# Kernel optimization log

Measured on AMD Instinct MI355X. Metric: run time of the kernel, lower is better.

## Reference

```python
import jax, jax.numpy as jnp
import numpy as np

B, E = 256, 65536          # batch, embed_dim
S = 256                    # seq_len = sqrt(E)
D = E // S                 # per-token input dim = 256
HID = 512                  # hidden_dim
HD = HID // 2              # per-direction GRU hidden = 256
GH = 128                   # gcn_hidden_dim
K = 5                      # k_neighbors


def setup_inputs() -> dict:
    key = jax.random.key(0)
    ks = jax.random.split(key, 16)
    s = 0.02
    return {
        "C_masked": jax.random.normal(ks[0], (B, E), jnp.float32),
        "W_proj": jax.random.normal(ks[1], (HID, D), jnp.float32) * s,
        "b_proj": jnp.zeros((HID,), jnp.float32),
        "Wih_f": jax.random.normal(ks[2], (3 * HD, HID), jnp.float32) * s,
        "Whh_f": jax.random.normal(ks[3], (3 * HD, HD), jnp.float32) * s,
        "bih_f": jnp.zeros((3 * HD,), jnp.float32),
        "bhh_f": jnp.zeros((3 * HD,), jnp.float32),
        "Wih_b": jax.random.normal(ks[4], (3 * HD, HID), jnp.float32) * s,
        "Whh_b": jax.random.normal(ks[5], (3 * HD, HD), jnp.float32) * s,
        "bih_b": jnp.zeros((3 * HD,), jnp.float32),
        "bhh_b": jnp.zeros((3 * HD,), jnp.float32),
        "W_gcn1": jax.random.normal(ks[6], (HID, GH), jnp.float32) * 0.01,
        "W_gcn2": jax.random.normal(ks[7], (GH, HID), jnp.float32) * 0.01,
    }


def _gru_dir(x, Wih, Whh, bih, bhh, reverse):
    # x: (B, S, IN) -> (B, S, HD). PyTorch GRU cell equations.
    gi = jnp.einsum('bsd,hd->bsh', x, Wih) + bih          # (B,S,3HD)
    gi = jnp.swapaxes(gi, 0, 1)                            # (S,B,3HD)
    h0 = jnp.zeros((x.shape[0], HD), x.dtype)

    def step(h, gi_t):
        gh = h @ Whh.T + bhh
        i_r, i_z, i_n = jnp.split(gi_t, 3, axis=-1)
        h_r, h_z, h_n = jnp.split(gh, 3, axis=-1)
        r = jax.nn.sigmoid(i_r + h_r)
        z = jax.nn.sigmoid(i_z + h_z)
        n = jnp.tanh(i_n + r * h_n)
        h_new = (1.0 - z) * n + z * h
        return h_new, h_new

    _, ys = jax.lax.scan(step, h0, gi, reverse=reverse)    # (S,B,HD), index-aligned
    return jnp.swapaxes(ys, 0, 1)


def reference(C_masked, W_proj, b_proj,
              Wih_f, Whh_f, bih_f, bhh_f,
              Wih_b, Whh_b, bih_b, bhh_b,
              W_gcn1, W_gcn2):
    b, e = C_masked.shape
    s = int(np.sqrt(e))
    d = e // s
    C_seq = C_masked.reshape(b, s, d)
    C_proj = jnp.einsum('bsd,hd->bsh', C_seq, W_proj) + b_proj   # (B,S,HID)

    # BiGRU (eval mode; dropout inactive)
    h_f = _gru_dir(C_proj, Wih_f, Whh_f, bih_f, bhh_f, reverse=False)
    h_b = _gru_dir(C_proj, Wih_b, Whh_b, bih_b, bhh_b, reverse=True)
    H = jnp.concatenate([h_f, h_b], axis=-1)                     # (B,S,HID)

    # KNN graph: cosine sim -> topk -> scatter 1.0 -> add self loops
    Hn = H / jnp.maximum(jnp.linalg.norm(H, axis=-1, keepdims=True), 1e-12)
    sim = jnp.einsum('bnd,bmd->bnm', Hn, Hn)                     # (B,S,S)
    topk_idx = jax.lax.top_k(sim, K)[1]                          # (B,S,K)
    bi = jnp.arange(b)[:, None, None]
    ni = jnp.arange(s)[None, :, None]
    A = jnp.zeros((b, s, s), H.dtype).at[bi, ni, topk_idx].set(1.0)
    A = A + jnp.eye(s, dtype=H.dtype)[None]

    # D^{-1/2} A D^{-1/2}
    deg = A.sum(axis=-1) + 1e-8
    dinv = deg ** -0.5
    A_norm = dinv[:, :, None] * A * dinv[:, None, :]

    # 2-layer GCN (dropout inactive in eval)
    Z1 = jax.nn.relu(jnp.einsum('bnm,bmh->bnh', A_norm, H @ W_gcn1))
    Z = jnp.einsum('bnm,bmh->bnh', A_norm, Z1 @ W_gcn2)
    return Z
```

## Files before the change

kernel.cpp:

```cpp
#include <hip/hip_runtime.h>
#include <hip/hip_fp16.h>
#include <cstdint>
#include <cmath>

typedef _Float16 f16x8 __attribute__((ext_vector_type(8)));
typedef float f32x4 __attribute__((ext_vector_type(4)));

#define MFMA16(A, B, C) __builtin_amdgcn_mfma_f32_16x16x32_f16(A, B, C, 0, 0, 0)
#define LO_SCALE 2048.0f
#define LO_INV   4.8828125e-4f

#define GBM 128
#define GBN 128
#define GBK 16

template<bool TRANSB>
__global__ __launch_bounds__(256)
void gemm_f32(int M, int N, int K,
              const float* __restrict__ A, long long sA,
              const float* __restrict__ B, long long sB,
              float* __restrict__ Cc, long long sC,
              const float* __restrict__ bias,
              const float* __restrict__ rsA,
              const float* __restrict__ rsB)
{
    const int z = blockIdx.z;
    A  += (size_t)z * (size_t)sA;
    B  += (size_t)z * (size_t)sB;
    Cc += (size_t)z * (size_t)sC;

    const int bm = blockIdx.y * GBM;
    const int bn = blockIdx.x * GBN;
    const int tid = threadIdx.x;
    const int tx = tid & 15;
    const int ty = tid >> 4;

    __shared__ float As[GBK][GBM + 4];
    __shared__ float Bs[GBK][GBN + 4];

    float acc[8][8];
#pragma unroll
    for (int i = 0; i < 8; ++i)
#pragma unroll
        for (int j = 0; j < 8; ++j) acc[i][j] = 0.0f;

    const int lr = tid >> 2;
    const int lk = (tid & 3) << 2;
    const int kb_n = tid >> 5;
    const int nb_n = (tid & 31) << 2;

    float sa0 = 1.f, sa1 = 1.f, sb0 = 1.f, sb1 = 1.f;
    if (rsA) {
        sa0 = rsA[(size_t)z * M + bm + lr];
        sa1 = rsA[(size_t)z * M + bm + lr + 64];
    }
    if (TRANSB && rsB) {
        sb0 = rsB[(size_t)z * N + bn + lr];
        sb1 = rsB[(size_t)z * N + bn + lr + 64];
    }

    float4 pa0, pa1, pb0, pb1;

    auto gload = [&](int kt) {
        const float* pA = A + (size_t)(bm + lr) * K + kt * GBK + lk;
        pa0 = *(const float4*)pA;
        pa1 = *(const float4*)(pA + (size_t)64 * K);
        if (TRANSB) {
            const float* pB = B + (size_t)(bn + lr) * K + kt * GBK + lk;
            pb0 = *(const float4*)pB;
            pb1 = *(const float4*)(pB + (size_t)64 * K);
        } else {
            const float* pB = B + (size_t)(kt * GBK + kb_n) * N + bn + nb_n;
            pb0 = *(const float4*)pB;
            pb1 = *(const float4*)(pB + (size_t)8 * N);
        }
    };
    auto sstore = [&]() {
        As[lk + 0][lr] = pa0.x * sa0; As[lk + 1][lr] = pa0.y * sa0;
        As[lk + 2][lr] = pa0.z * sa0; As[lk + 3][lr] = pa0.w * sa0;
        As[lk + 0][lr + 64] = pa1.x * sa1; As[lk + 1][lr + 64] = pa1.y * sa1;
        As[lk + 2][lr + 64] = pa1.z * sa1; As[lk + 3][lr + 64] = pa1.w * sa1;
        if (TRANSB) {
            Bs[lk + 0][lr] = pb0.x * sb0; Bs[lk + 1][lr] = pb0.y * sb0;
            Bs[lk + 2][lr] = pb0.z * sb0; Bs[lk + 3][lr] = pb0.w * sb0;
            Bs[lk + 0][lr + 64] = pb1.x * sb1; Bs[lk + 1][lr + 64] = pb1.y * sb1;
            Bs[lk + 2][lr + 64] = pb1.z * sb1; Bs[lk + 3][lr + 64] = pb1.w * sb1;
        } else {
            *(float4*)&Bs[kb_n][nb_n]     = pb0;
            *(float4*)&Bs[kb_n + 8][nb_n] = pb1;
        }
    };

    const int nkt = K / GBK;
    gload(0);
    sstore();
    __syncthreads();
    for (int kt = 0; kt < nkt; ++kt) {
        if (kt + 1 < nkt) gload(kt + 1);
#pragma unroll
        for (int k = 0; k < GBK; ++k) {
            float4 a0 = *(const float4*)&As[k][ty * 8];
            float4 a1 = *(const float4*)&As[k][ty * 8 + 4];
            float4 b0 = *(const float4*)&Bs[k][tx * 8];
            float4 b1 = *(const float4*)&Bs[k][tx * 8 + 4];
            float av[8] = {a0.x, a0.y, a0.z, a0.w, a1.x, a1.y, a1.z, a1.w};
            float bv[8] = {b0.x, b0.y, b0.z, b0.w, b1.x, b1.y, b1.z, b1.w};
#pragma unroll
            for (int i = 0; i < 8; ++i)
#pragma unroll
                for (int j = 0; j < 8; ++j)
                    acc[i][j] = fmaf(av[i], bv[j], acc[i][j]);
        }
        __syncthreads();
        if (kt + 1 < nkt) { sstore(); __syncthreads(); }
    }

    float bb[8];
#pragma unroll
    for (int j = 0; j < 8; ++j) bb[j] = bias ? bias[bn + tx * 8 + j] : 0.0f;
#pragma unroll
    for (int i = 0; i < 8; ++i) {
        const int row = bm + ty * 8 + i;
        float* cp = Cc + (size_t)row * N + bn + tx * 8;
        float4 o0 = make_float4(acc[i][0] + bb[0], acc[i][1] + bb[1],
                                acc[i][2] + bb[2], acc[i][3] + bb[3]);
        float4 o1 = make_float4(acc[i][4] + bb[4], acc[i][5] + bb[5],
                                acc[i][6] + bb[6], acc[i][7] + bb[7]);
        *(float4*)cp = o0;
        *(float4*)(cp + 4) = o1;
    }
}

__global__ void bias_combine(const float* __restrict__ Wih, const float* __restrict__ b_proj,
                             const float* __restrict__ bih, float* __restrict__ bcomb)
{
    const int j = blockIdx.x * blockDim.x + threadIdx.x;
    if (j >= 768) return;
    float s = bih[j];
    for (int k = 0; k < 512; ++k) s = fmaf(Wih[(size_t)j * 512 + k], b_proj[k], s);
    bcomb[j] = s;
}

__global__ __launch_bounds__(256)
void pack_w(const float* __restrict__ W, unsigned short* __restrict__ pack)
{
    const int idx = blockIdx.x * 256 + threadIdx.x;
    if (idx >= 768 * 256) return;
    const int n = idx >> 8;
    const int k = idx & 255;
    const float w = W[idx];
    const __half hi = __float2half(w);
    const __half lo = __float2half((w - __half2float(hi)) * LO_SCALE);
    const int nt = n >> 4;
    const int lane = ((k >> 3) & 3) * 16 + (n & 15);
    const int j = k & 7;
    const int kc = k >> 5;
    const size_t base = ((size_t)(nt * 8 + kc) * 2) * 512 + lane * 8 + j;
    pack[base]       = __half_as_ushort(hi);
    pack[base + 512] = __half_as_ushort(lo);
}

__global__ __launch_bounds__(256)
void pack_bk(const float* __restrict__ W, unsigned short* __restrict__ pack,
             int K, int N)
{
    const int idx = blockIdx.x * 256 + threadIdx.x;
    if (idx >= K * N) return;
    const int k = idx / N;
    const int n = idx - k * N;
    const float w = W[idx];
    const __half hi = __float2half(w);
    const __half lo = __float2half((w - __half2float(hi)) * LO_SCALE);
    const int nt = n >> 4;
    const int kc = k >> 5;
    const int lane = ((k >> 3) & 3) * 16 + (n & 15);
    const int j = k & 7;
    const int KC = K >> 5;
    const size_t base = ((size_t)(nt * KC + kc) * 2) * 512 + lane * 8 + j;
    pack[base]       = __half_as_ushort(hi);
    pack[base + 512] = __half_as_ushort(lo);
}

__global__ __launch_bounds__(512)
void gi_gemm_c(const float* __restrict__ Cm, const unsigned short* __restrict__ pack,
               const float* __restrict__ bcomb, float* __restrict__ gi, int t0)
{
    const int tid = threadIdx.x;
    const int w = tid >> 6, l = tid & 63;
    const int l15 = l & 15, l4 = l >> 4;
    const int bgrp = blockIdx.x >> 1;
    const int half = blockIdx.x & 1;
    const size_t m0 = (size_t)bgrp * 256 + t0 + half * 64;
    const size_t o0 = (size_t)bgrp * 128 + half * 64;

    __shared__ unsigned short alds[2][64 * 256];

    {
        const int row = tid >> 3;
        const int seg = (tid & 7) * 32;
        const float4* src = (const float4*)(Cm + (m0 + row) * 256 + seg);
        const int sw = (row & 7) << 3;
#pragma unroll
        for (int i = 0; i < 8; ++i) {
            float4 v = src[i];
            float vv[4] = {v.x, v.y, v.z, v.w};
#pragma unroll
            for (int e = 0; e < 4; ++e) {
                const float x = vv[e];
                const __half hi = __float2half(x);
                const __half lo = __float2half((x - __half2float(hi)) * LO_SCALE);
                const int ad = (row << 8) + ((seg + i * 4 + e) ^ sw);
                alds[0][ad] = __half_as_ushort(hi);
                alds[1][ad] = __half_as_ushort(lo);
            }
        }
    }
    __syncthreads();

    const int mt = w >> 1, nh = w & 1;
    f32x4 acc[24];
#pragma unroll
    for (int i = 0; i < 24; ++i) acc[i] = (f32x4){0.f, 0.f, 0.f, 0.f};

    const int ar = mt * 16 + l15;
    const int arow = ar << 8;
    const int asw = (ar & 7) << 3;

#pragma unroll
    for (int kc = 0; kc < 8; ++kc) {
        const int ad = arow + ((kc * 32 + l4 * 8) ^ asw);
        const f16x8 ahi = *(const f16x8*)&alds[0][ad];
        const f16x8 alo = *(const f16x8*)&alds[1][ad];
#pragma unroll
        for (int nt = 0; nt < 24; ++nt) {
            const int nt_lin = nh * 24 + nt;
            const uint4* bp = (const uint4*)(pack + ((size_t)(nt_lin * 8 + kc) * 2) * 512);
            uint4 bh4 = bp[l];
            uint4 bl4 = bp[64 + l];
            const f16x8 Bhi = *reinterpret_cast<const f16x8*>(&bh4);
            const f16x8 Blo = *reinterpret_cast<const f16x8*>(&bl4);
            acc[nt] = MFMA16(ahi, Bhi, acc[nt]);
            f32x4 t2 = (f32x4){0.f, 0.f, 0.f, 0.f};
            t2 = MFMA16(ahi, Blo, t2);
            t2 = MFMA16(alo, Bhi, t2);
#pragma unroll
            for (int r = 0; r < 4; ++r) acc[nt][r] = fmaf(LO_INV, t2[r], acc[nt][r]);
        }
    }

#pragma unroll
    for (int nt = 0; nt < 24; ++nt) {
        const int n = (nh * 24 + nt) * 16 + l15;
        const float bb = bcomb[n];
#pragma unroll
        for (int r = 0; r < 4; ++r) {
            const size_t om = o0 + mt * 16 + l4 * 4 + r;
            __builtin_nontemporal_store(acc[nt][r] + bb, &gi[om * 768 + n]);
        }
    }
}

__global__ __launch_bounds__(1024)
void gru_scan_v8(const float* __restrict__ gi_fc, const float* __restrict__ gi_bc,
                 const float* __restrict__ Whh_f, const float* __restrict__ Whh_b,
                 const float* __restrict__ bhh_f, const float* __restrict__ bhh_b,
                 float* __restrict__ H, float* __restrict__ hstate, int phase)
{
    const int bid = blockIdx.x;
    const int xcd = bid & 7;
    const int dir = xcd >> 2;
    const int grp = (bid >> 3) * 4 + (xcd & 3);
    const float* __restrict__ gi  = dir ? gi_bc : gi_fc;
    const float* __restrict__ Whh = dir ? Whh_b : Whh_f;
    const float* __restrict__ bhh = dir ? bhh_b : bhh_f;
    const int b0 = grp * 4;
    const int t0 = dir ? (128 - phase * 128) : (phase * 128);

    const int tid = threadIdx.x;
    const int j = tid >> 2;
    const int q = tid & 3;

    __shared__ float hb[2][4][256];

    float hreg = (phase == 0)
        ? 0.0f
        : hstate[((size_t)dir * 256 + b0 + q) * 256 + j];
    hb[0][q][j] = hreg;

    const float bh_r = bhh[j], bh_z = bhh[j + 256], bh_n = bhh[j + 512];

    const float* __restrict__ Wr = Whh + (size_t)j * 256 + q * 4;
    const float* __restrict__ Wz = Whh + (size_t)(j + 256) * 256 + q * 4;
    const float* __restrict__ Wn = Whh + (size_t)(j + 512) * 256 + q * 4;

    __syncthreads();

    int p = 0;
    for (int tau = 0; tau < 128; ++tau) {
        const int sc = dir ? (127 - tau) : tau;
        const int tt = t0 + sc;

        const float* gp = gi + ((size_t)(b0 + q) * 128 + sc) * 768 + j;
        const float g_r = __builtin_nontemporal_load(gp);
        const float g_z = __builtin_nontemporal_load(gp + 256);
        const float g_n = __builtin_nontemporal_load(gp + 512);

        float ar0 = 0.f, ar1 = 0.f, ar2 = 0.f, ar3 = 0.f;
        float az0 = 0.f, az1 = 0.f, az2 = 0.f, az3 = 0.f;
        float an0 = 0.f, an1 = 0.f, an2 = 0.f, an3 = 0.f;
#pragma unroll
        for (int u = 0; u < 16; ++u) {
            const float4 wr = *(const float4*)(Wr + u * 16);
            const float4 wz = *(const float4*)(Wz + u * 16);
            const float4 wn = *(const float4*)(Wn + u * 16);
            const int ha = u * 16 + q * 4;
            const float4 h0 = *(const float4*)&hb[p][0][ha];
            const float4 h1 = *(const float4*)&hb[p][1][ha];
            const float4 h2 = *(const float4*)&hb[p][2][ha];
            const float4 h3 = *(const float4*)&hb[p][3][ha];
            ar0 = fmaf(wr.x, h0.x, ar0); ar0 = fmaf(wr.y, h0.y, ar0);
            ar0 = fmaf(wr.z, h0.z, ar0); ar0 = fmaf(wr.w, h0.w, ar0);
            ar1 = fmaf(wr.x, h1.x, ar1); ar1 = fmaf(wr.y, h1.y, ar1);
            ar1 = fmaf(wr.z, h1.z, ar1); ar1 = fmaf(wr.w, h1.w, ar1);
            ar2 = fmaf(wr.x, h2.x, ar2); ar2 = fmaf(wr.y, h2.y, ar2);
            ar2 = fmaf(wr.z, h2.z, ar2); ar2 = fmaf(wr.w, h2.w, ar2);
            ar3 = fmaf(wr.x, h3.x, ar3); ar3 = fmaf(wr.y, h3.y, ar3);
            ar3 = fmaf(wr.z, h3.z, ar3); ar3 = fmaf(wr.w, h3.w, ar3);
            az0 = fmaf(wz.x, h0.x, az0); az0 = fmaf(wz.y, h0.y, az0);
            az0 = fmaf(wz.z, h0.z, az0); az0 = fmaf(wz.w, h0.w, az0);
            az1 = fmaf(wz.x, h1.x, az1); az1 = fmaf(wz.y, h1.y, az1);
            az1 = fmaf(wz.z, h1.z, az1); az1 = fmaf(wz.w, h1.w, az1);
            az2 = fmaf(wz.x, h2.x, az2); az2 = fmaf(wz.y, h2.y, az2);
            az2 = fmaf(wz.z, h2.z, az2); az2 = fmaf(wz.w, h2.w, az2);
            az3 = fmaf(wz.x, h3.x, az3); az3 = fmaf(wz.y, h3.y, az3);
            az3 = fmaf(wz.z, h3.z, az3); az3 = fmaf(wz.w, h3.w, az3);
            an0 = fmaf(wn.x, h0.x, an0); an0 = fmaf(wn.y, h0.y, an0);
            an0 = fmaf(wn.z, h0.z, an0); an0 = fmaf(wn.w, h0.w, an0);
            an1 = fmaf(wn.x, h1.x, an1); an1 = fmaf(wn.y, h1.y, an1);
            an1 = fmaf(wn.z, h1.z, an1); an1 = fmaf(wn.w, h1.w, an1);
            an2 = fmaf(wn.x, h2.x, an2); an2 = fmaf(wn.y, h2.y, an2);
            an2 = fmaf(wn.z, h2.z, an2); an2 = fmaf(wn.w, h2.w, an2);
            an3 = fmaf(wn.x, h3.x, an3); an3 = fmaf(wn.y, h3.y, an3);
            an3 = fmaf(wn.z, h3.z, an3); an3 = fmaf(wn.w, h3.w, an3);
        }

        ar0 += __shfl_xor(ar0, 1); ar0 += __shfl_xor(ar0, 2);
        ar1 += __shfl_xor(ar1, 1); ar1 += __shfl_xor(ar1, 2);
        ar2 += __shfl_xor(ar2, 1); ar2 += __shfl_xor(ar2, 2);
        ar3 += __shfl_xor(ar3, 1); ar3 += __shfl_xor(ar3, 2);
        az0 += __shfl_xor(az0, 1); az0 += __shfl_xor(az0, 2);
        az1 += __shfl_xor(az1, 1); az1 += __shfl_xor(az1, 2);
        az2 += __shfl_xor(az2, 1); az2 += __shfl_xor(az2, 2);
        az3 += __shfl_xor(az3, 1); az3 += __shfl_xor(az3, 2);
        an0 += __shfl_xor(an0, 1); an0 += __shfl_xor(an0, 2);
        an1 += __shfl_xor(an1, 1); an1 += __shfl_xor(an1, 2);
        an2 += __shfl_xor(an2, 1); an2 += __shfl_xor(an2, 2);
        an3 += __shfl_xor(an3, 1); an3 += __shfl_xor(an3, 2);

        const float pr = (q == 0) ? ar0 : (q == 1) ? ar1 : (q == 2) ? ar2 : ar3;
        const float pz = (q == 0) ? az0 : (q == 1) ? az1 : (q == 2) ? az2 : az3;
        const float pn = (q == 0) ? an0 : (q == 1) ? an1 : (q == 2) ? an2 : an3;

        const float rr = 1.0f / (1.0f + expf(-(g_r + pr + bh_r)));
        const float zz = 1.0f / (1.0f + expf(-(g_z + pz + bh_z)));
        const float nn = tanhf(g_n + rr * (pn + bh_n));
        hreg = (1.0f - zz) * nn + zz * hreg;

        hb[p ^ 1][q][j] = hreg;
        __builtin_nontemporal_store(
            hreg, &H[((size_t)(b0 + q) * 256 + tt) * 512 + dir * 256 + j]);
        __syncthreads();
        p ^= 1;
    }

    hstate[((size_t)dir * 256 + b0 + q) * 256 + j] = hreg;
}

__global__ __launch_bounds__(256)
void rownorm(const float* __restrict__ H, float* __restrict__ rinv)
{
    const int row  = blockIdx.x * 4 + (threadIdx.x >> 6);
    const int lane = threadIdx.x & 63;
    const float4* p = (const float4*)(H + (size_t)row * 512);
    float ss = 0.f;
    float4 v = p[lane];
    ss += v.x * v.x + v.y * v.y + v.z * v.z + v.w * v.w;
    v = p[lane + 64];
    ss += v.x * v.x + v.y * v.y + v.z * v.z + v.w * v.w;
#pragma unroll
    for (int off = 32; off >= 1; off >>= 1) ss += __shfl_xor(ss, off);
    if (lane == 0) rinv[row] = 1.0f / fmaxf(sqrtf(ss), 1e-12f);
}

__global__ __launch_bounds__(512)
void sim_mfma(const float* __restrict__ H, const float* __restrict__ rinv,
              float* __restrict__ sim)
{
    const int b = blockIdx.x;
    const int tid = threadIdx.x;
    const int w = tid >> 6, l = tid & 63;
    const int l15 = l & 15, l4 = l >> 4;

    __shared__ unsigned short st[2][256][40];

    f32x4 acc[2][16];
#pragma unroll
    for (int m = 0; m < 2; ++m)
#pragma unroll
        for (int n = 0; n < 16; ++n) acc[m][n] = (f32x4){0.f, 0.f, 0.f, 0.f};

    const int sr = tid >> 1;
    const int sh = (tid & 1) * 16;
    const float rv = rinv[b * 256 + sr];
    const float* hrow = H + ((size_t)b * 256 + sr) * 512;

    for (int kc = 0; kc < 16; ++kc) {
        if (kc) __syncthreads();
        {
            const float4* src = (const float4*)(hrow + kc * 32 + sh);
#pragma unroll
            for (int i = 0; i < 4; ++i) {
                float4 v = src[i];
                float vv[4] = {v.x, v.y, v.z, v.w};
                ushort4 h4, l4v;
                unsigned short* hp = (unsigned short*)&h4;
                unsigned short* lp = (unsigned short*)&l4v;
#pragma unroll
                for (int e = 0; e < 4; ++e) {
                    const float x = vv[e] * rv;
                    const __half hi = __float2half(x);
                    const __half lo = __float2half((x - __half2float(hi)) * LO_SCALE);
                    hp[e] = __half_as_ushort(hi);
                    lp[e] = __half_as_ushort(lo);
                }
                *(ushort4*)&st[0][sr][sh + i * 4] = h4;
                *(ushort4*)&st[1][sr][sh + i * 4] = l4v;
            }
        }
        __syncthreads();

        f16x8 ahi[2], alo[2];
#pragma unroll
        for (int m = 0; m < 2; ++m) {
            const int row = (w * 2 + m) * 16 + l15;
            ahi[m] = *(const f16x8*)&st[0][row][l4 * 8];
            alo[m] = *(const f16x8*)&st[1][row][l4 * 8];
        }
#pragma unroll
        for (int nt = 0; nt < 16; ++nt) {
            const int col = nt * 16 + l15;
            const f16x8 bhi = *(const f16x8*)&st[0][col][l4 * 8];
            const f16x8 blo = *(const f16x8*)&st[1][col][l4 * 8];
#pragma unroll
            for (int m = 0; m < 2; ++m) {
                acc[m][nt] = MFMA16(ahi[m], bhi, acc[m][nt]);
                f32x4 t2 = (f32x4){0.f, 0.f, 0.f, 0.f};
                t2 = MFMA16(ahi[m], blo, t2);
                t2 = MFMA16(alo[m], bhi, t2);
#pragma unroll
                for (int r = 0; r < 4; ++r)
                    acc[m][nt][r] = fmaf(LO_INV, t2[r], acc[m][nt][r]);
            }
        }
    }

#pragma unroll
    for (int m = 0; m < 2; ++m) {
        const int row0 = (w * 2 + m) * 16 + l4 * 4;
#pragma unroll
        for (int nt = 0; nt < 16; ++nt)
#pragma unroll
            for (int r = 0; r < 4; ++r)
                sim[((size_t)b * 256 + row0 + r) * 256 + nt * 16 + l15] = acc[m][nt][r];
    }
}

template<int KDIM, int NDIM, int NT_PER>
__global__ __launch_bounds__(512)
void gcn_mm(const float* __restrict__ X, const unsigned short* __restrict__ pack,
            float* __restrict__ Y)
{
    const int tid = threadIdx.x;
    const int w = tid >> 6, l = tid & 63;
    const int l15 = l & 15, l4 = l >> 4;
    const int m0 = blockIdx.x * 64;
    constexpr int KC = KDIM / 32;

    __shared__ unsigned short a[2][64 * KDIM];

    {
        const int row = tid >> 3;
        const int seg = (tid & 7) * (KDIM / 8);
        const float4* src = (const float4*)(X + (size_t)(m0 + row) * KDIM + seg);
        const int sw = (row & 7) << 3;
#pragma unroll
        for (int i = 0; i < KDIM / 32; ++i) {
            float4 v = src[i];
            float vv[4] = {v.x, v.y, v.z, v.w};
#pragma unroll
            for (int e = 0; e < 4; ++e) {
                const float x = vv[e];
                const __half hi = __float2half(x);
                const __half lo = __float2half((x - __half2float(hi)) * LO_SCALE);
                const int ad = row * KDIM + ((seg + i * 4 + e) ^ sw);
                a[0][ad] = __half_as_ushort(hi);
                a[1][ad] = __half_as_ushort(lo);
            }
        }
    }
    __syncthreads();

    const int mt = w >> 1, nh = w & 1;
    f32x4 acc[NT_PER];
#pragma unroll
    for (int i = 0; i < NT_PER; ++i) acc[i] = (f32x4){0.f, 0.f, 0.f, 0.f};

    const int arow = mt * 16 + l15;
    const int abase = arow * KDIM;
    const int asw = (arow & 7) << 3;

#pragma unroll
    for (int kc = 0; kc < KC; ++kc) {
        const int ad = abase + ((kc * 32 + l4 * 8) ^ asw);
        const f16x8 ahi = *(const f16x8*)&a[0][ad];
        const f16x8 alo = *(const f16x8*)&a[1][ad];
#pragma unroll
        for (int ntl = 0; ntl < NT_PER; ++ntl) {
            const int nt = nh * NT_PER + ntl;
            const uint4* bp = (const uint4*)(pack + ((size_t)(nt * KC + kc) * 2) * 512);
            uint4 bh4 = bp[l];
            uint4 bl4 = bp[64 + l];
            const f16x8 Bhi = *reinterpret_cast<const f16x8*>(&bh4);
            const f16x8 Blo = *reinterpret_cast<const f16x8*>(&bl4);
            acc[ntl] = MFMA16(ahi, Bhi, acc[ntl]);
            f32x4 t2 = (f32x4){0.f, 0.f, 0.f, 0.f};
            t2 = MFMA16(ahi, Blo, t2);
            t2 = MFMA16(alo, Bhi, t2);
#pragma unroll
            for (int r = 0; r < 4; ++r) acc[ntl][r] = fmaf(LO_INV, t2[r], acc[ntl][r]);
        }
    }

#pragma unroll
    for (int ntl = 0; ntl < NT_PER; ++ntl) {
        const int n = (nh * NT_PER + ntl) * 16 + l15;
#pragma unroll
        for (int r = 0; r < 4; ++r) {
            const int m = m0 + mt * 16 + l4 * 4 + r;
            Y[(size_t)m * NDIM + n] = acc[ntl][r];
        }
    }
}

__global__ __launch_bounds__(256)
void topk5(const float* __restrict__ sim, int* __restrict__ idx)
{
    const int row = blockIdx.x * 256 + threadIdx.x;
    const float* p = sim + (size_t)row * 256;
    float bv0 = -1e30f, bv1 = -1e30f, bv2 = -1e30f, bv3 = -1e30f, bv4 = -1e30f;
    int   bi0 = 0, bi1 = 0, bi2 = 0, bi3 = 0, bi4 = 0;
    for (int m4 = 0; m4 < 64; ++m4) {
        float4 v4 = *(const float4*)(p + m4 * 4);
        float vv[4] = {v4.x, v4.y, v4.z, v4.w};
#pragma unroll
        for (int c = 0; c < 4; ++c) {
            float v = vv[c];
            int   m = m4 * 4 + c;
            if (v > bv0) {
                if (v > bv1) {
                    bv0 = bv1; bi0 = bi1;
                    if (v > bv2) {
                        bv1 = bv2; bi1 = bi2;
                        if (v > bv3) {
                            bv2 = bv3; bi2 = bi3;
                            if (v > bv4) { bv3 = bv4; bi3 = bi4; bv4 = v; bi4 = m; }
                            else         { bv3 = v;  bi3 = m; }
                        } else { bv2 = v; bi2 = m; }
                    } else { bv1 = v; bi1 = m; }
                } else { bv0 = v; bi0 = m; }
            }
        }
    }
    int* o = idx + (size_t)row * 5;
    o[0] = bi0; o[1] = bi1; o[2] = bi2; o[3] = bi3; o[4] = bi4;
}

template<bool RELU, int DIM>
__global__ __launch_bounds__(128)
void gcn_agg(const float* __restrict__ X, const int* __restrict__ idxs,
             float* __restrict__ outp, float cnorm)
{
    const int row = blockIdx.x;
    const int bbase = row & ~255;
    const int* id = idxs + (size_t)row * 5;
    const int i0 = bbase + id[0];
    const int i1 = bbase + id[1];
    const int i2 = bbase + id[2];
    const int i3 = bbase + id[3];
    const int i4 = bbase + id[4];
    const int t = threadIdx.x;
    if (DIM == 512) {
        const float4* Xp = (const float4*)X;
        float4 a = Xp[(size_t)row * 128 + t];
        float4 v;
        v = Xp[(size_t)i0 * 128 + t]; a.x += v.x; a.y += v.y; a.z += v.z; a.w += v.w;
        v = Xp[(size_t)i1 * 128 + t]; a.x += v.x; a.y += v.y; a.z += v.z; a.w += v.w;
        v = Xp[(size_t)i2 * 128 + t]; a.x += v.x; a.y += v.y; a.z += v.z; a.w += v.w;
        v = Xp[(size_t)i3 * 128 + t]; a.x += v.x; a.y += v.y; a.z += v.z; a.w += v.w;
        v = Xp[(size_t)i4 * 128 + t]; a.x += v.x; a.y += v.y; a.z += v.z; a.w += v.w;
        a.x *= cnorm; a.y *= cnorm; a.z *= cnorm; a.w *= cnorm;
        if (RELU) {
            a.x = fmaxf(a.x, 0.f); a.y = fmaxf(a.y, 0.f);
            a.z = fmaxf(a.z, 0.f); a.w = fmaxf(a.w, 0.f);
        }
        ((float4*)outp)[(size_t)row * 128 + t] = a;
    } else {
        float a = X[(size_t)row * 128 + t];
        a += X[(size_t)i0 * 128 + t];
        a += X[(size_t)i1 * 128 + t];
        a += X[(size_t)i2 * 128 + t];
        a += X[(size_t)i3 * 128 + t];
        a += X[(size_t)i4 * 128 + t];
        a *= cnorm;
        if (RELU) a = fmaxf(a, 0.f);
        outp[(size_t)row * 128 + t] = a;
    }
}

extern "C" void kernel_launch(void* const* d_in, const int* in_sizes, int n_in,
                              void* d_out, int out_size, void* d_ws, size_t ws_size,
                              hipStream_t stream)
{
    (void)in_sizes; (void)n_in; (void)out_size; (void)ws_size;

    const float* C_masked = (const float*)d_in[0];
    const float* W_proj   = (const float*)d_in[1];
    const float* b_proj   = (const float*)d_in[2];
    const float* Wih_f    = (const float*)d_in[3];
    const float* Whh_f    = (const float*)d_in[4];
    const float* bih_f    = (const float*)d_in[5];
    const float* bhh_f    = (const float*)d_in[6];
    const float* Wih_b    = (const float*)d_in[7];
    const float* Whh_b    = (const float*)d_in[8];
    const float* bih_b    = (const float*)d_in[9];
    const float* bhh_b    = (const float*)d_in[10];
    const float* W_gcn1   = (const float*)d_in[11];
    const float* W_gcn2   = (const float*)d_in[12];
    float* out = (float*)d_out;

    char* ws = (char*)d_ws;
    size_t o = 0;
    auto take = [&](size_t bytes) {
        size_t r = o;
        o = (o + bytes + 255) & ~(size_t)255;
        return r;
    };
    const size_t WCOMB_B = (size_t)768 * 256 * 4;
    const size_t PACK_B  = (size_t)48 * 8 * 2 * 512 * 2;
    const size_t PACKG_B = (size_t)262144;
    const size_t o_wcf  = take(WCOMB_B);
    const size_t o_wcb  = take(WCOMB_B);
    const size_t o_bcf  = take(768 * 4);
    const size_t o_bcb  = take(768 * 4);
    const size_t o_rinv = take((size_t)65536 * 4);
    const size_t o_topk = take((size_t)65536 * 5 * 4);
    const size_t o_pwf  = take(PACK_B);
    const size_t o_pwb  = take(PACK_B);
    const size_t o_pg1  = take(PACKG_B);
    const size_t o_pg2  = take(PACKG_B);
    const size_t o_hst  = take((size_t)512 * 256 * 4);
    const size_t regionA = o;

    const size_t GIC_BYTES = (size_t)256 * 128 * 768 * 4;
    const size_t H_BYTES   = (size_t)65536 * 512 * 4;

    float* wcomb_f = (float*)(ws + o_wcf);
    float* wcomb_b = (float*)(ws + o_wcb);
    float* bcomb_f = (float*)(ws + o_bcf);
    float* bcomb_b = (float*)(ws + o_bcb);
    float* rinv    = (float*)(ws + o_rinv);
    int*   topk    = (int*)(ws + o_topk);
    unsigned short* packWf = (unsigned short*)(ws + o_pwf);
    unsigned short* packWb = (unsigned short*)(ws + o_pwb);
    unsigned short* packG1 = (unsigned short*)(ws + o_pg1);
    unsigned short* packG2 = (unsigned short*)(ws + o_pg2);
    float* hstate = (float*)(ws + o_hst);

    float* gi_fc = (float*)(ws + regionA);
    float* gi_bc = (float*)(ws + regionA + GIC_BYTES);
    float* Hbuf  = (float*)(ws + regionA + 2 * GIC_BYTES);

    float* sim  = (float*)(ws + regionA);
    float* XW1  = (float*)(ws + regionA + 67108864);
    float* Z1   = (float*)(ws + regionA + 100663296);
    float* Z1W2 = (float*)(ws + regionA);

    const dim3 blk(256);

    gemm_f32<false><<<dim3(2, 6, 1), blk, 0, stream>>>(
        768, 256, 512, Wih_f, 0, W_proj, 0, wcomb_f, 0, nullptr, nullptr, nullptr);
    gemm_f32<false><<<dim3(2, 6, 1), blk, 0, stream>>>(
        768, 256, 512, Wih_b, 0, W_proj, 0, wcomb_b, 0, nullptr, nullptr, nullptr);
    bias_combine<<<3, 256, 0, stream>>>(Wih_f, b_proj, bih_f, bcomb_f);
    bias_combine<<<3, 256, 0, stream>>>(Wih_b, b_proj, bih_b, bcomb_b);
    pack_w<<<768, 256, 0, stream>>>(wcomb_f, packWf);
    pack_w<<<768, 256, 0, stream>>>(wcomb_b, packWb);
    pack_bk<<<256, 256, 0, stream>>>(W_gcn1, packG1, 512, 128);
    pack_bk<<<256, 256, 0, stream>>>(W_gcn2, packG2, 128, 512);

    gi_gemm_c<<<512, 512, 0, stream>>>(C_masked, packWf, bcomb_f, gi_fc, 0);
    gi_gemm_c<<<512, 512, 0, stream>>>(C_masked, packWb, bcomb_b, gi_bc, 128);
    gru_scan_v8<<<128, 1024, 0, stream>>>(gi_fc, gi_bc, Whh_f, Whh_b,
                                          bhh_f, bhh_b, Hbuf, hstate, 0);
    gi_gemm_c<<<512, 512, 0, stream>>>(C_masked, packWf, bcomb_f, gi_fc, 128);
    gi_gemm_c<<<512, 512, 0, stream>>>(C_masked, packWb, bcomb_b, gi_bc, 0);
    gru_scan_v8<<<128, 1024, 0, stream>>>(gi_fc, gi_bc, Whh_f, Whh_b,
                                          bhh_f, bhh_b, Hbuf, hstate, 1);

    rownorm<<<16384, blk, 0, stream>>>(Hbuf, rinv);
    sim_mfma<<<256, 512, 0, stream>>>(Hbuf, rinv, sim);
    topk5<<<256, blk, 0, stream>>>(sim, topk);

    const float cnorm = (float)(1.0 / (6.0 + 1e-8));
    gcn_mm<512, 128, 4><<<1024, 512, 0, stream>>>(Hbuf, packG1, XW1);
    gcn_agg<true, 128><<<65536, 128, 0, stream>>>(XW1, topk, Z1, cnorm);
    gcn_mm<128, 512, 16><<<1024, 512, 0, stream>>>(Z1, packG2, Z1W2);
    gcn_agg<false, 512><<<65536, 128, 0, stream>>>(Z1W2, topk, out, cnorm);
}
```

Before: 5.988 ms.

## Process eight batch rows per GRU scan block to reuse recurrent weight loads

The GRU recurrence kernel now handles 8 batch rows per block instead of 4, halving the grid to 64 blocks, so each Whh weight load from memory/cache is reused across twice as many hidden-state rows. Weight loads are also software-pipelined three iterations ahead through a small rotating register buffer. This cuts weight-load traffic per step but doubles per-thread accumulators and FMA work, raising register pressure, and uses only 64 of the available CUs.

```diff
diff --git a/kernel.cpp b/kernel.cpp
--- a/kernel.cpp
+++ b/kernel.cpp
@@ -261,7 +261,7 @@
 }
 
 __global__ __launch_bounds__(1024)
-void gru_scan_v8(const float* __restrict__ gi_fc, const float* __restrict__ gi_bc,
+void gru_scan_v9(const float* __restrict__ gi_fc, const float* __restrict__ gi_bc,
                  const float* __restrict__ Whh_f, const float* __restrict__ Whh_b,
                  const float* __restrict__ bhh_f, const float* __restrict__ bhh_b,
                  float* __restrict__ H, float* __restrict__ hstate, int phase)
@@ -273,22 +273,26 @@
     const float* __restrict__ gi  = dir ? gi_bc : gi_fc;
     const float* __restrict__ Whh = dir ? Whh_b : Whh_f;
     const float* __restrict__ bhh = dir ? bhh_b : bhh_f;
-    const int b0 = grp * 4;
+    const int b0 = grp * 8;
     const int t0 = dir ? (128 - phase * 128) : (phase * 128);
 
     const int tid = threadIdx.x;
     const int j = tid >> 2;
     const int q = tid & 3;
-
-    __shared__ float hb[2][4][256];
-
-    float hreg = (phase == 0)
-        ? 0.0f
-        : hstate[((size_t)dir * 256 + b0 + q) * 256 + j];
-    hb[0][q][j] = hreg;
+    const int bA = q, bB = q + 4;
+
+    __shared__ float hb[2][8][256];
+
+    float hregA, hregB;
+    if (phase == 0) { hregA = 0.f; hregB = 0.f; }
+    else {
+        hregA = hstate[((size_t)dir * 256 + b0 + bA) * 256 + j];
+        hregB = hstate[((size_t)dir * 256 + b0 + bB) * 256 + j];
+    }
+    hb[0][bA][j] = hregA;
+    hb[0][bB][j] = hregB;
 
     const float bh_r = bhh[j], bh_z = bhh[j + 256], bh_n = bhh[j + 512];
-
     const float* __restrict__ Wr = Whh + (size_t)j * 256 + q * 4;
     const float* __restrict__ Wz = Whh + (size_t)(j + 256) * 256 + q * 4;
     const float* __restrict__ Wn = Whh + (size_t)(j + 512) * 256 + q * 4;
@@ -300,80 +304,84 @@
         const int sc = dir ? (127 - tau) : tau;
         const int tt = t0 + sc;
 
-        const float* gp = gi + ((size_t)(b0 + q) * 128 + sc) * 768 + j;
-        const float g_r = __builtin_nontemporal_load(gp);
-        const float g_z = __builtin_nontemporal_load(gp + 256);
-        const float g_n = __builtin_nontemporal_load(gp + 512);
-
-        float ar0 = 0.f, ar1 = 0.f, ar2 = 0.f, ar3 = 0.f;
-        float az0 = 0.f, az1 = 0.f, az2 = 0.f, az3 = 0.f;
-        float an0 = 0.f, an1 = 0.f, an2 = 0.f, an3 = 0.f;
+        const float* gpA = gi + ((size_t)(b0 + bA) * 128 + sc) * 768 + j;
+        const float* gpB = gi + ((size_t)(b0 + bB) * 128 + sc) * 768 + j;
+        const float grA = __builtin_nontemporal_load(gpA);
+        const float gzA = __builtin_nontemporal_load(gpA + 256);
+        const float gnA = __builtin_nontemporal_load(gpA + 512);
+        const float grB = __builtin_nontemporal_load(gpB);
+        const float gzB = __builtin_nontemporal_load(gpB + 256);
+        const float gnB = __builtin_nontemporal_load(gpB + 512);
+
+        float ar[8], az[8], an[8];
+#pragma unroll
+        for (int b = 0; b < 8; ++b) { ar[b] = 0.f; az[b] = 0.f; an[b] = 0.f; }
+
+        float4 wrP[3], wzP[3], wnP[3];
+#pragma unroll
+        for (int i = 0; i < 3; ++i) {
+            wrP[i] = *(const float4*)(Wr + i * 16);
+            wzP[i] = *(const float4*)(Wz + i * 16);
+            wnP[i] = *(const float4*)(Wn + i * 16);
+        }
+
 #pragma unroll
         for (int u = 0; u < 16; ++u) {
-            const float4 wr = *(const float4*)(Wr + u * 16);
-            const float4 wz = *(const float4*)(Wz + u * 16);
-            const float4 wn = *(const float4*)(Wn + u * 16);
+            const int s3 = u % 3;
+            const float4 wr = wrP[s3], wz = wzP[s3], wn = wnP[s3];
+            if (u + 3 < 16) {
+                wrP[s3] = *(const float4*)(Wr + (u + 3) * 16);
+                wzP[s3] = *(const float4*)(Wz + (u + 3) * 16);
+                wnP[s3] = *(const float4*)(Wn + (u + 3) * 16);
+            }
             const int ha = u * 16 + q * 4;
-            const float4 h0 = *(const float4*)&hb[p][0][ha];
-            const float4 h1 = *(const float4*)&hb[p][1][ha];
-            const float4 h2 = *(const float4*)&hb[p][2][ha];
-            const float4 h3 = *(const float4*)&hb[p][3][ha];
-            ar0 = fmaf(wr.x, h0.x, ar0); ar0 = fmaf(wr.y, h0.y, ar0);
-            ar0 = fmaf(wr.z, h0.z, ar0); ar0 = fmaf(wr.w, h0.w, ar0);
-            ar1 = fmaf(wr.x, h1.x, ar1); ar1 = fmaf(wr.y, h1.y, ar1);
-            ar1 = fmaf(wr.z, h1.z, ar1); ar1 = fmaf(wr.w, h1.w, ar1);
-            ar2 = fmaf(wr.x, h2.x, ar2); ar2 = fmaf(wr.y, h2.y, ar2);
-            ar2 = fmaf(wr.z, h2.z, ar2); ar2 = fmaf(wr.w, h2.w, ar2);
-            ar3 = fmaf(wr.x, h3.x, ar3); ar3 = fmaf(wr.y, h3.y, ar3);
-            ar3 = fmaf(wr.z, h3.z, ar3); ar3 = fmaf(wr.w, h3.w, ar3);
-            az0 = fmaf(wz.x, h0.x, az0); az0 = fmaf(wz.y, h0.y, az0);
-            az0 = fmaf(wz.z, h0.z, az0); az0 = fmaf(wz.w, h0.w, az0);
-            az1 = fmaf(wz.x, h1.x, az1); az1 = fmaf(wz.y, h1.y, az1);
-            az1 = fmaf(wz.z, h1.z, az1); az1 = fmaf(wz.w, h1.w, az1);
-            az2 = fmaf(wz.x, h2.x, az2); az2 = fmaf(wz.y, h2.y, az2);
-            az2 = fmaf(wz.z, h2.z, az2); az2 = fmaf(wz.w, h2.w, az2);
-            az3 = fmaf(wz.x, h3.x, az3); az3 = fmaf(wz.y, h3.y, az3);
-            az3 = fmaf(wz.z, h3.z, az3); az3 = fmaf(wz.w, h3.w, az3);
-            an0 = fmaf(wn.x, h0.x, an0); an0 = fmaf(wn.y, h0.y, an0);
-            an0 = fmaf(wn.z, h0.z, an0); an0 = fmaf(wn.w, h0.w, an0);
-            an1 = fmaf(wn.x, h1.x, an1); an1 = fmaf(wn.y, h1.y, an1);
-            an1 = fmaf(wn.z, h1.z, an1); an1 = fmaf(wn.w, h1.w, an1);
-            an2 = fmaf(wn.x, h2.x, an2); an2 = fmaf(wn.y, h2.y, an2);
-            an2 = fmaf(wn.z, h2.z, an2); an2 = fmaf(wn.w, h2.w, an2);
-            an3 = fmaf(wn.x, h3.x, an3); an3 = fmaf(wn.y, h3.y, an3);
-            an3 = fmaf(wn.z, h3.z, an3); an3 = fmaf(wn.w, h3.w, an3);
-        }
-
-        ar0 += __shfl_xor(ar0, 1); ar0 += __shfl_xor(ar0, 2);
-        ar1 += __shfl_xor(ar1, 1); ar1 += __shfl_xor(ar1, 2);
-        ar2 += __shfl_xor(ar2, 1); ar2 += __shfl_xor(ar2, 2);
-        ar3 += __shfl_xor(ar3, 1); ar3 += __shfl_xor(ar3, 2);
-        az0 += __shfl_xor(az0, 1); az0 += __shfl_xor(az0, 2);
-        az1 += __shfl_xor(az1, 1); az1 += __shfl_xor(az1, 2);
-        az2 += __shfl_xor(az2, 1); az2 += __shfl_xor(az2, 2);
-        az3 += __shfl_xor(az3, 1); az3 += __shfl_xor(az3, 2);
-        an0 += __shfl_xor(an0, 1); an0 += __shfl_xor(an0, 2);
-        an1 += __shfl_xor(an1, 1); an1 += __shfl_xor(an1, 2);
-        an2 += __shfl_xor(an2, 1); an2 += __shfl_xor(an2, 2);
-        an3 += __shfl_xor(an3, 1); an3 += __shfl_xor(an3, 2);
-
-        const float pr = (q == 0) ? ar0 : (q == 1) ? ar1 : (q == 2) ? ar2 : ar3;
-        const float pz = (q == 0) ? az0 : (q == 1) ? az1 : (q == 2) ? az2 : az3;
-        const float pn = (q == 0) ? an0 : (q == 1) ? an1 : (q == 2) ? an2 : an3;
-
-        const float rr = 1.0f / (1.0f + expf(-(g_r + pr + bh_r)));
-        const float zz = 1.0f / (1.0f + expf(-(g_z + pz + bh_z)));
-        const float nn = tanhf(g_n + rr * (pn + bh_n));
-        hreg = (1.0f - zz) * nn + zz * hreg;
-
-        hb[p ^ 1][q][j] = hreg;
+#pragma unroll
+            for (int b = 0; b < 8; ++b) {
+                const float4 hv = *(const float4*)&hb[p][b][ha];
+                ar[b] = fmaf(wr.x, hv.x, ar[b]); ar[b] = fmaf(wr.y, hv.y, ar[b]);
+                ar[b] = fmaf(wr.z, hv.z, ar[b]); ar[b] = fmaf(wr.w, hv.w, ar[b]);
+                az[b] = fmaf(wz.x, hv.x, az[b]); az[b] = fmaf(wz.y, hv.y, az[b]);
+                az[b] = fmaf(wz.z, hv.z, az[b]); az[b] = fmaf(wz.w, hv.w, az[b]);
+                an[b] = fmaf(wn.x, hv.x, an[b]); an[b] = fmaf(wn.y, hv.y, an[b]);
+                an[b] = fmaf(wn.z, hv.z, an[b]); an[b] = fmaf(wn.w, hv.w, an[b]);
+            }
+        }
+
+#pragma unroll
+        for (int b = 0; b < 8; ++b) {
+            ar[b] += __shfl_xor(ar[b], 1); ar[b] += __shfl_xor(ar[b], 2);
+            az[b] += __shfl_xor(az[b], 1); az[b] += __shfl_xor(az[b], 2);
+            an[b] += __shfl_xor(an[b], 1); an[b] += __shfl_xor(an[b], 2);
+        }
+
+        const float prA = (q == 0) ? ar[0] : (q == 1) ? ar[1] : (q == 2) ? ar[2] : ar[3];
+        const float pzA = (q == 0) ? az[0] : (q == 1) ? az[1] : (q == 2) ? az[2] : az[3];
+        const float pnA = (q == 0) ? an[0] : (q == 1) ? an[1] : (q == 2) ? an[2] : an[3];
+        const float prB = (q == 0) ? ar[4] : (q == 1) ? ar[5] : (q == 2) ? ar[6] : ar[7];
+        const float pzB = (q == 0) ? az[4] : (q == 1) ? az[5] : (q == 2) ? az[6] : az[7];
+        const float pnB = (q == 0) ? an[4] : (q == 1) ? an[5] : (q == 2) ? an[6] : an[7];
+
+        float rr = 1.0f / (1.0f + expf(-(grA + prA + bh_r)));
+        float zz = 1.0f / (1.0f + expf(-(gzA + pzA + bh_z)));
+        float nn = tanhf(gnA + rr * (pnA + bh_n));
+        hregA = (1.0f - zz) * nn + zz * hregA;
+        rr = 1.0f / (1.0f + expf(-(grB + prB + bh_r)));
+        zz = 1.0f / (1.0f + expf(-(gzB + pzB + bh_z)));
+        nn = tanhf(gnB + rr * (pnB + bh_n));
+        hregB = (1.0f - zz) * nn + zz * hregB;
+
+        hb[p ^ 1][bA][j] = hregA;
+        hb[p ^ 1][bB][j] = hregB;
         __builtin_nontemporal_store(
-            hreg, &H[((size_t)(b0 + q) * 256 + tt) * 512 + dir * 256 + j]);
+            hregA, &H[((size_t)(b0 + bA) * 256 + tt) * 512 + dir * 256 + j]);
+        __builtin_nontemporal_store(
+            hregB, &H[((size_t)(b0 + bB) * 256 + tt) * 512 + dir * 256 + j]);
         __syncthreads();
         p ^= 1;
     }
 
-    hstate[((size_t)dir * 256 + b0 + q) * 256 + j] = hreg;
+    hstate[((size_t)dir * 256 + b0 + bA) * 256 + j] = hregA;
+    hstate[((size_t)dir * 256 + b0 + bB) * 256 + j] = hregB;
 }
 
 __global__ __launch_bounds__(256)
@@ -672,7 +680,6 @@
     const size_t regionA = o;
 
     const size_t GIC_BYTES = (size_t)256 * 128 * 768 * 4;
-    const size_t H_BYTES   = (size_t)65536 * 512 * 4;
 
     float* wcomb_f = (float*)(ws + o_wcf);
     float* wcomb_b = (float*)(ws + o_wcb);
@@ -710,12 +717,12 @@
 
     gi_gemm_c<<<512, 512, 0, stream>>>(C_masked, packWf, bcomb_f, gi_fc, 0);
     gi_gemm_c<<<512, 512, 0, stream>>>(C_masked, packWb, bcomb_b, gi_bc, 128);
-    gru_scan_v8<<<128, 1024, 0, stream>>>(gi_fc, gi_bc, Whh_f, Whh_b,
-                                          bhh_f, bhh_b, Hbuf, hstate, 0);
+    gru_scan_v9<<<64, 1024, 0, stream>>>(gi_fc, gi_bc, Whh_f, Whh_b,
+                                         bhh_f, bhh_b, Hbuf, hstate, 0);
     gi_gemm_c<<<512, 512, 0, stream>>>(C_masked, packWf, bcomb_f, gi_fc, 128);
     gi_gemm_c<<<512, 512, 0, stream>>>(C_masked, packWb, bcomb_b, gi_bc, 0);
-    gru_scan_v8<<<128, 1024, 0, stream>>>(gi_fc, gi_bc, Whh_f, Whh_b,
-                                          bhh_f, bhh_b, Hbuf, hstate, 1);
+    gru_scan_v9<<<64, 1024, 0, stream>>>(gi_fc, gi_bc, Whh_f, Whh_b,
+                                         bhh_f, bhh_b, Hbuf, hstate, 1);
 
     rownorm<<<16384, blk, 0, stream>>>(Hbuf, rinv);
     sim_mfma<<<256, 512, 0, stream>>>(Hbuf, rinv, sim);
```

Result: slower. 6.763 ms (+12.9%).

## Repack recurrent GRU weights for coalesced loads and prefetch next-step gate inputs

Applied to the files above, without the earlier changes.

Adds a packing kernel that reorders Whh so that, at each unroll step, the 1024 threads of the GRU scan read consecutive float4s. Before this, each thread read a strided row segment. The scan also loads the next timestep's input-gate values one iteration early to hide global latency behind the recurrent matvec. A launch-bounds occupancy hint is added as well. The cost is one extra packed weight buffer per direction and two small pack launches.

```diff
diff --git a/kernel.cpp b/kernel.cpp
--- a/kernel.cpp
+++ b/kernel.cpp
@@ -181,6 +181,21 @@
     pack[base + 512] = __half_as_ushort(lo);
 }
 
+__global__ __launch_bounds__(256)
+void pack_wsc(const float* __restrict__ W, float* __restrict__ wpk)
+{
+    const int idx = blockIdx.x * 256 + threadIdx.x;
+    if (idx >= 768 * 256) return;
+    const int row = idx >> 8;
+    const int k   = idx & 255;
+    const int g = row >> 8;
+    const int j = row & 255;
+    const int u = k >> 4;
+    const int q = (k >> 2) & 3;
+    const int e = k & 3;
+    wpk[(((size_t)(u * 3 + g) * 1024) + (j << 2) + q) * 4 + e] = W[idx];
+}
+
 __global__ __launch_bounds__(512)
 void gi_gemm_c(const float* __restrict__ Cm, const unsigned short* __restrict__ pack,
                const float* __restrict__ bcomb, float* __restrict__ gi, int t0)
@@ -260,18 +275,18 @@
     }
 }
 
-__global__ __launch_bounds__(1024)
-void gru_scan_v8(const float* __restrict__ gi_fc, const float* __restrict__ gi_bc,
-                 const float* __restrict__ Whh_f, const float* __restrict__ Whh_b,
-                 const float* __restrict__ bhh_f, const float* __restrict__ bhh_b,
-                 float* __restrict__ H, float* __restrict__ hstate, int phase)
+__global__ __launch_bounds__(1024, 4)
+void gru_scan_v11(const float* __restrict__ gi_fc, const float* __restrict__ gi_bc,
+                  const float* __restrict__ wpk_f, const float* __restrict__ wpk_b,
+                  const float* __restrict__ bhh_f, const float* __restrict__ bhh_b,
+                  float* __restrict__ H, float* __restrict__ hstate, int phase)
 {
     const int bid = blockIdx.x;
     const int xcd = bid & 7;
     const int dir = xcd >> 2;
     const int grp = (bid >> 3) * 4 + (xcd & 3);
     const float* __restrict__ gi  = dir ? gi_bc : gi_fc;
-    const float* __restrict__ Whh = dir ? Whh_b : Whh_f;
+    const float4* __restrict__ Wp = (const float4*)(dir ? wpk_b : wpk_f);
     const float* __restrict__ bhh = dir ? bhh_b : bhh_f;
     const int b0 = grp * 4;
     const int t0 = dir ? (128 - phase * 128) : (phase * 128);
@@ -289,30 +304,38 @@
 
     const float bh_r = bhh[j], bh_z = bhh[j + 256], bh_n = bhh[j + 512];
 
-    const float* __restrict__ Wr = Whh + (size_t)j * 256 + q * 4;
-    const float* __restrict__ Wz = Whh + (size_t)(j + 256) * 256 + q * 4;
-    const float* __restrict__ Wn = Whh + (size_t)(j + 512) * 256 + q * 4;
-
     __syncthreads();
+
+    int sc0 = dir ? 127 : 0;
+    {
+    }
+    const float* gp0 = gi + ((size_t)(b0 + q) * 128 + sc0) * 768 + j;
+    float gpr = __builtin_nontemporal_load(gp0);
+    float gpz = __builtin_nontemporal_load(gp0 + 256);
+    float gpn = __builtin_nontemporal_load(gp0 + 512);
 
     int p = 0;
     for (int tau = 0; tau < 128; ++tau) {
         const int sc = dir ? (127 - tau) : tau;
         const int tt = t0 + sc;
 
-        const float* gp = gi + ((size_t)(b0 + q) * 128 + sc) * 768 + j;
-        const float g_r = __builtin_nontemporal_load(gp);
-        const float g_z = __builtin_nontemporal_load(gp + 256);
-        const float g_n = __builtin_nontemporal_load(gp + 512);
+        const float g_r = gpr, g_z = gpz, g_n = gpn;
+        if (tau < 127) {
+            const int scn = dir ? (126 - tau) : (tau + 1);
+            const float* gq = gi + ((size_t)(b0 + q) * 128 + scn) * 768 + j;
+            gpr = __builtin_nontemporal_load(gq);
+            gpz = __builtin_nontemporal_load(gq + 256);
+            gpn = __builtin_nontemporal_load(gq + 512);
+        }
 
         float ar0 = 0.f, ar1 = 0.f, ar2 = 0.f, ar3 = 0.f;
         float az0 = 0.f, az1 = 0.f, az2 = 0.f, az3 = 0.f;
         float an0 = 0.f, an1 = 0.f, an2 = 0.f, an3 = 0.f;
 #pragma unroll
         for (int u = 0; u < 16; ++u) {
-            const float4 wr = *(const float4*)(Wr + u * 16);
-            const float4 wz = *(const float4*)(Wz + u * 16);
-            const float4 wn = *(const float4*)(Wn + u * 16);
+            const float4 wr = Wp[(u * 3 + 0) * 1024 + tid];
+            const float4 wz = Wp[(u * 3 + 1) * 1024 + tid];
+            const float4 wn = Wp[(u * 3 + 2) * 1024 + tid];
             const int ha = u * 16 + q * 4;
             const float4 h0 = *(const float4*)&hb[p][0][ha];
             const float4 h1 = *(const float4*)&hb[p][1][ha];
@@ -666,13 +689,14 @@
     const size_t o_topk = take((size_t)65536 * 5 * 4);
     const size_t o_pwf  = take(PACK_B);
     const size_t o_pwb  = take(PACK_B);
+    const size_t o_wsf  = take(WCOMB_B);
+    const size_t o_wsb  = take(WCOMB_B);
     const size_t o_pg1  = take(PACKG_B);
     const size_t o_pg2  = take(PACKG_B);
     const size_t o_hst  = take((size_t)512 * 256 * 4);
     const size_t regionA = o;
 
     const size_t GIC_BYTES = (size_t)256 * 128 * 768 * 4;
-    const size_t H_BYTES   = (size_t)65536 * 512 * 4;
 
     float* wcomb_f = (float*)(ws + o_wcf);
     float* wcomb_b = (float*)(ws + o_wcb);
@@ -682,6 +706,8 @@
     int*   topk    = (int*)(ws + o_topk);
     unsigned short* packWf = (unsigned short*)(ws + o_pwf);
     unsigned short* packWb = (unsigned short*)(ws + o_pwb);
+    float* wpkF = (float*)(ws + o_wsf);
+    float* wpkB = (float*)(ws + o_wsb);
     unsigned short* packG1 = (unsigned short*)(ws + o_pg1);
     unsigned short* packG2 = (unsigned short*)(ws + o_pg2);
     float* hstate = (float*)(ws + o_hst);
@@ -705,17 +731,19 @@
     bias_combine<<<3, 256, 0, stream>>>(Wih_b, b_proj, bih_b, bcomb_b);
     pack_w<<<768, 256, 0, stream>>>(wcomb_f, packWf);
     pack_w<<<768, 256, 0, stream>>>(wcomb_b, packWb);
+    pack_wsc<<<768, 256, 0, stream>>>(Whh_f, wpkF);
+    pack_wsc<<<768, 256, 0, stream>>>(Whh_b, wpkB);
     pack_bk<<<256, 256, 0, stream>>>(W_gcn1, packG1, 512, 128);
     pack_bk<<<256, 256, 0, stream>>>(W_gcn2, packG2, 128, 512);
 
     gi_gemm_c<<<512, 512, 0, stream>>>(C_masked, packWf, bcomb_f, gi_fc, 0);
     gi_gemm_c<<<512, 512, 0, stream>>>(C_masked, packWb, bcomb_b, gi_bc, 128);
-    gru_scan_v8<<<128, 1024, 0, stream>>>(gi_fc, gi_bc, Whh_f, Whh_b,
-                                          bhh_f, bhh_b, Hbuf, hstate, 0);
+    gru_scan_v11<<<128, 1024, 0, stream>>>(gi_fc, gi_bc, wpkF, wpkB,
+                                           bhh_f, bhh_b, Hbuf, hstate, 0);
     gi_gemm_c<<<512, 512, 0, stream>>>(C_masked, packWf, bcomb_f, gi_fc, 128);
     gi_gemm_c<<<512, 512, 0, stream>>>(C_masked, packWb, bcomb_b, gi_bc, 0);
-    gru_scan_v8<<<128, 1024, 0, stream>>>(gi_fc, gi_bc, Whh_f, Whh_b,
-                                          bhh_f, bhh_b, Hbuf, hstate, 1);
+    gru_scan_v11<<<128, 1024, 0, stream>>>(gi_fc, gi_bc, wpkF, wpkB,
+                                           bhh_f, bhh_b, Hbuf, hstate, 1);
 
     rownorm<<<16384, blk, 0, stream>>>(Hbuf, rinv);
     sim_mfma<<<256, 512, 0, stream>>>(Hbuf, rinv, sim);
```

Measured after the change: 6.287 ms. 5.0% more time.
